# Performance work log

Measured on AMD Instinct MI355X. Metric: run time of the kernel, lower is better.

## Reference

```python
import jax, jax.numpy as jnp
import numpy as np

EMBED_DIM = 512
NUM_HEADS = 8
HEAD_DIM = EMBED_DIM // NUM_HEADS
FFN_DIM = 4 * EMBED_DIM
B, S = 4, 2048
LN_EPS = 1e-5


def _linear_params(key, fan_in, fan_out):
    kw, kb = jax.random.split(key)
    bound = 1.0 / np.sqrt(fan_in)
    W = jax.random.uniform(kw, (fan_in, fan_out), jnp.float32, -bound, bound)
    b = jax.random.uniform(kb, (fan_out,), jnp.float32, -bound, bound)
    return W, b


def setup_inputs() -> dict:
    key = jax.random.key(0)
    ks = jax.random.split(key, 10)
    query = jax.random.normal(ks[0], (B, S, EMBED_DIM), jnp.float32)
    key_t = jax.random.normal(ks[1], (B, S, EMBED_DIM), jnp.float32)
    value = jax.random.normal(ks[2], (B, S, EMBED_DIM), jnp.float32)
    Wq, bq = _linear_params(ks[3], EMBED_DIM, EMBED_DIM)
    Wk, bk = _linear_params(ks[4], EMBED_DIM, EMBED_DIM)
    Wv, bv = _linear_params(ks[5], EMBED_DIM, EMBED_DIM)
    Wo, bo = _linear_params(ks[6], EMBED_DIM, EMBED_DIM)
    W1, b1 = _linear_params(ks[7], EMBED_DIM, FFN_DIM)
    W2, b2 = _linear_params(ks[8], FFN_DIM, EMBED_DIM)
    g1 = jnp.ones((EMBED_DIM,), jnp.float32); be1 = jnp.zeros((EMBED_DIM,), jnp.float32)
    g2 = jnp.ones((EMBED_DIM,), jnp.float32); be2 = jnp.zeros((EMBED_DIM,), jnp.float32)
    return dict(query=query, key=key_t, value=value,
                Wq=Wq, bq=bq, Wk=Wk, bk=bk, Wv=Wv, bv=bv, Wo=Wo, bo=bo,
                g1=g1, be1=be1, g2=g2, be2=be2,
                W1=W1, b1=b1, W2=W2, b2=b2)


def _layernorm(x, g, b):
    mu = jnp.mean(x, axis=-1, keepdims=True)
    var = jnp.mean(jnp.square(x - mu), axis=-1, keepdims=True)
    return (x - mu) * jax.lax.rsqrt(var + LN_EPS) * g + b


def reference(query, key, value, Wq, bq, Wk, bk, Wv, bv, Wo, bo,
              g1, be1, g2, be2, W1, b1, W2, b2):
    b_, s_ = query.shape[:2]
    # projections -> [B, H, S, Dh]
    Q = (query @ Wq + bq).reshape(b_, -1, NUM_HEADS, HEAD_DIM).transpose(0, 2, 1, 3)
    K = (key @ Wk + bk).reshape(b_, -1, NUM_HEADS, HEAD_DIM).transpose(0, 2, 1, 3)
    V = (value @ Wv + bv).reshape(b_, -1, NUM_HEADS, HEAD_DIM).transpose(0, 2, 1, 3)
    scores = jnp.einsum('bhqd,bhkd->bhqk', Q, K) / jnp.sqrt(jnp.float32(HEAD_DIM))
    attn = jax.nn.softmax(scores, axis=-1)  # dropout is eval-mode identity
    ctx = jnp.einsum('bhqk,bhkd->bhqd', attn, V)
    ctx = ctx.transpose(0, 2, 1, 3).reshape(b_, -1, EMBED_DIM)
    out = ctx @ Wo + bo
    out = _layernorm(query + out, g1, be1)
    ffn = jax.nn.gelu(out @ W1 + b1, approximate=False) @ W2 + b2
    return _layernorm(out + ffn, g2, be2)
```

## Files before the change

### kernel.cpp

```cpp
#include <hip/hip_runtime.h>
#include <hip/hip_bf16.h>
#include <math.h>

#define EMBED 512
#define NHEAD 8
#define HDIM 64
#define FFN 2048
#define BB 4
#define SS 2048
#define MROWS (BB*SS)
#define NB ((size_t)MROWS * EMBED)
#define LN_EPS 1e-5f

typedef __attribute__((ext_vector_type(8))) short short8;
typedef __attribute__((ext_vector_type(4))) float floatx4;

__device__ inline float bf2f(__hip_bfloat16 x) { return __bfloat162float(x); }
__device__ inline __hip_bfloat16 f2bf(float x) { return __float2bfloat16(x); }

__device__ inline float gelu_f(float x) {
    return 0.5f * x * (1.0f + erff(x * 0.70710678118654752f));
}

__device__ inline void async_copy16(const void* g, void* l) {
    __builtin_amdgcn_global_load_lds(
        (const __attribute__((address_space(1))) void*)g,
        (__attribute__((address_space(3))) void*)l, 16, 0, 0);
}

__global__ void detect_kernel(const void* __restrict__ q, int* __restrict__ flag) {
    const float* qf = (const float*)q;
    int lane = threadIdx.x;
    float v = qf[lane * 1024 + 7];
    bool ok = (v == v) && (fabsf(v) > 0x1p-40f) && (fabsf(v) < 0x1p40f);
    unsigned long long m = __ballot(ok);
    if (lane == 0) *flag = (__popcll(m) >= 32) ? 1 : 0;
}

__global__ __launch_bounds__(256) void cvt_qkv_kernel(
    const void* __restrict__ q, const void* __restrict__ k, const void* __restrict__ v,
    __hip_bfloat16* __restrict__ out, const int* __restrict__ dflag)
{
    const int f32 = *dflag;
    size_t pos = ((size_t)blockIdx.x * 256 + threadIdx.x) * 8;
    int sel = (int)(pos >> 22);
    size_t off = pos & (NB - 1);
    const void* src = sel == 0 ? q : sel == 1 ? k : v;
    if (f32) {
        const float* s = (const float*)src + off;
        float4 f0 = *reinterpret_cast<const float4*>(s);
        float4 f1 = *reinterpret_cast<const float4*>(s + 4);
        alignas(16) __hip_bfloat16 h[8] = {
            f2bf(f0.x), f2bf(f0.y), f2bf(f0.z), f2bf(f0.w),
            f2bf(f1.x), f2bf(f1.y), f2bf(f1.z), f2bf(f1.w)};
        *reinterpret_cast<uint4*>(out + pos) = *reinterpret_cast<const uint4*>(h);
    } else {
        *reinterpret_cast<uint4*>(out + pos) =
            *reinterpret_cast<const uint4*>((const __hip_bfloat16*)src + off);
    }
}

__global__ __launch_bounds__(256) void transpose_tile_kernel(
    const void* __restrict__ src, __hip_bfloat16* __restrict__ dst,
    int R, int C, const int* __restrict__ dflag)
{
    const int f32 = *dflag;
    const int r0 = blockIdx.x * 64, c0 = blockIdx.y * 64;
    __shared__ __hip_bfloat16 L[64][65];
    const int t = threadIdx.x;
    for (int c = t; c < 4096; c += 256) {
        int lr = c >> 6, lc = c & 63;
        __hip_bfloat16 v = f32 ? f2bf(((const float*)src)[(size_t)(r0 + lr) * C + c0 + lc])
                               : ((const __hip_bfloat16*)src)[(size_t)(r0 + lr) * C + c0 + lc];
        L[lr][lc] = v;
    }
    __syncthreads();
    for (int c = t; c < 4096; c += 256) {
        int lr = c >> 6, lc = c & 63;
        dst[(size_t)(c0 + lr) * R + r0 + lc] = L[lc][lr];
    }
}

__global__ __launch_bounds__(256) void transpose_tile4_kernel(
    const void* __restrict__ s0, const void* __restrict__ s1,
    const void* __restrict__ s2, const void* __restrict__ s3,
    __hip_bfloat16* __restrict__ dbase,
    const int* __restrict__ dflag)
{
    const int f32 = *dflag;
    const int which = blockIdx.z;
    const void* src = which == 0 ? s0 : which == 1 ? s1 : which == 2 ? s2 : s3;
    __hip_bfloat16* dst = dbase + (size_t)which * 512 * 512;
    const int r0 = blockIdx.x * 64, c0 = blockIdx.y * 64;
    __shared__ __hip_bfloat16 L[64][65];
    const int t = threadIdx.x;
    for (int c = t; c < 4096; c += 256) {
        int lr = c >> 6, lc = c & 63;
        __hip_bfloat16 v = f32 ? f2bf(((const float*)src)[(size_t)(r0 + lr) * 512 + c0 + lc])
                               : ((const __hip_bfloat16*)src)[(size_t)(r0 + lr) * 512 + c0 + lc];
        L[lr][lc] = v;
    }
    __syncthreads();
    for (int c = t; c < 4096; c += 256) {
        int lr = c >> 6, lc = c & 63;
        dst[(size_t)(c0 + lr) * 512 + r0 + lc] = L[lc][lr];
    }
}

template<int ACT, int BIAS>
__global__ __launch_bounds__(256) void gemm_bt_lds_kernel(
    const __hip_bfloat16* __restrict__ A,
    const __hip_bfloat16* __restrict__ Bt,
    const void* __restrict__ bias,
    __hip_bfloat16* __restrict__ C,
    int M, int N, int K, int ksplit, const int* __restrict__ dflag)
{
    const int f32 = *dflag;
    const int bm = blockIdx.x * 128;
    const int bn = blockIdx.y * 128;
    int kbeg = 0, kend = K;
    if (BIAS == 0) {
        kbeg = blockIdx.z * ksplit;
        kend = kbeg + ksplit;
        C += (size_t)blockIdx.z * NB;
    }
    const int t = threadIdx.x;
    const int wave = t >> 6, lane = t & 63;
    const int wm = (wave >> 1) * 64, wn = (wave & 1) * 64;
    const int quad = lane >> 4, r = lane & 15;

    __shared__ alignas(16) __hip_bfloat16 As[128 * 32];
    __shared__ alignas(16) __hip_bfloat16 Bs[128 * 32];

    floatx4 acc[4][4];
    #pragma unroll
    for (int i = 0; i < 4; ++i)
        #pragma unroll
        for (int j = 0; j < 4; ++j)
            acc[i][j] = (floatx4){0.f, 0.f, 0.f, 0.f};

    const int c0 = wave * 128;

    for (int kt = kbeg; kt < kend; kt += 32) {
        #pragma unroll
        for (int it = 0; it < 2; ++it) {
            int c = c0 + it * 64 + lane;
            int row = c >> 2, col = (c & 3) * 8;
            async_copy16(A + (size_t)(bm + row) * K + kt + col,
                         As + (size_t)(c0 + it * 64) * 8);
            async_copy16(Bt + (size_t)(bn + row) * K + kt + col,
                         Bs + (size_t)(c0 + it * 64) * 8);
        }
        __syncthreads();
        short8 af[4], bfr[4];
        #pragma unroll
        for (int i = 0; i < 4; ++i)
            af[i] = *reinterpret_cast<const short8*>(&As[(wm + i * 16 + r) * 32 + quad * 8]);
        #pragma unroll
        for (int j = 0; j < 4; ++j)
            bfr[j] = *reinterpret_cast<const short8*>(&Bs[(wn + j * 16 + r) * 32 + quad * 8]);
        #pragma unroll
        for (int i = 0; i < 4; ++i)
            #pragma unroll
            for (int j = 0; j < 4; ++j)
                acc[i][j] = __builtin_amdgcn_mfma_f32_16x16x32_bf16(af[i], bfr[j], acc[i][j], 0, 0, 0);
        __syncthreads();
    }

    #pragma unroll
    for (int j = 0; j < 4; ++j) {
        const int n = bn + wn + j * 16 + r;
        float bvv = 0.f;
        if (BIAS) bvv = f32 ? ((const float*)bias)[n]
                            : bf2f(((const __hip_bfloat16*)bias)[n]);
        #pragma unroll
        for (int i = 0; i < 4; ++i) {
            #pragma unroll
            for (int v = 0; v < 4; ++v) {
                int m = bm + wm + i * 16 + quad * 4 + v;
                float x = acc[i][j][v] + bvv;
                if (ACT == 1) x = gelu_f(x);
                C[(size_t)m * N + n] = f2bf(x);
            }
        }
    }
}

__global__ __launch_bounds__(256) void gemm_qkv_fused_kernel(
    const __hip_bfloat16* __restrict__ Acat,
    const __hip_bfloat16* __restrict__ Wcat,
    const void* __restrict__ bq, const void* __restrict__ bk, const void* __restrict__ bv,
    __hip_bfloat16* __restrict__ Ocat,
    const int* __restrict__ dflag)
{
    const int f32 = *dflag;
    const int sel = blockIdx.x >> 6;
    const __hip_bfloat16* A = Acat + (size_t)sel * NB;
    const __hip_bfloat16* Bt = Wcat + (size_t)sel * 512 * 512;
    const void* bias = sel == 0 ? bq : sel == 1 ? bk : bv;
    __hip_bfloat16* C = Ocat + (size_t)sel * NB;

    const int bm = (blockIdx.x & 63) * 128;
    const int bn = blockIdx.y * 128;
    const int t = threadIdx.x;
    const int wave = t >> 6, lane = t & 63;
    const int wm = (wave >> 1) * 64, wn = (wave & 1) * 64;
    const int quad = lane >> 4, r = lane & 15;
    const int K = EMBED, N = EMBED;

    __shared__ alignas(16) __hip_bfloat16 As[128 * 32];
    __shared__ alignas(16) __hip_bfloat16 Bs[128 * 32];

    floatx4 acc[4][4];
    #pragma unroll
    for (int i = 0; i < 4; ++i)
        #pragma unroll
        for (int j = 0; j < 4; ++j)
            acc[i][j] = (floatx4){0.f, 0.f, 0.f, 0.f};

    const int c0 = wave * 128;

    for (int kt = 0; kt < K; kt += 32) {
        #pragma unroll
        for (int it = 0; it < 2; ++it) {
            int c = c0 + it * 64 + lane;
            int row = c >> 2, col = (c & 3) * 8;
            async_copy16(A + (size_t)(bm + row) * K + kt + col,
                         As + (size_t)(c0 + it * 64) * 8);
            async_copy16(Bt + (size_t)(bn + row) * K + kt + col,
                         Bs + (size_t)(c0 + it * 64) * 8);
        }
        __syncthreads();
        short8 af[4], bfr[4];
        #pragma unroll
        for (int i = 0; i < 4; ++i)
            af[i] = *reinterpret_cast<const short8*>(&As[(wm + i * 16 + r) * 32 + quad * 8]);
        #pragma unroll
        for (int j = 0; j < 4; ++j)
            bfr[j] = *reinterpret_cast<const short8*>(&Bs[(wn + j * 16 + r) * 32 + quad * 8]);
        #pragma unroll
        for (int i = 0; i < 4; ++i)
            #pragma unroll
            for (int j = 0; j < 4; ++j)
                acc[i][j] = __builtin_amdgcn_mfma_f32_16x16x32_bf16(af[i], bfr[j], acc[i][j], 0, 0, 0);
        __syncthreads();
    }

    #pragma unroll
    for (int j = 0; j < 4; ++j) {
        const int n = bn + wn + j * 16 + r;
        const float bvv = f32 ? ((const float*)bias)[n]
                              : bf2f(((const __hip_bfloat16*)bias)[n]);
        #pragma unroll
        for (int i = 0; i < 4; ++i) {
            #pragma unroll
            for (int v = 0; v < 4; ++v) {
                int m = bm + wm + i * 16 + quad * 4 + v;
                C[(size_t)m * N + n] = f2bf(acc[i][j][v] + bvv);
            }
        }
    }
}

__global__ __launch_bounds__(256) void vtrans_kernel(
    const __hip_bfloat16* __restrict__ Vb, __hip_bfloat16* __restrict__ Vt)
{
    const int bh = blockIdx.y;
    const int b = bh >> 3, h = bh & 7;
    const int s0 = blockIdx.x * 64;
    __shared__ alignas(16) __hip_bfloat16 L[64][72];
    const int t = threadIdx.x;
    for (int c = t; c < 512; c += 256) {
        int row = c >> 3, g = c & 7;
        *reinterpret_cast<uint4*>(&L[row][g * 8]) =
            *reinterpret_cast<const uint4*>(Vb + (size_t)(b * SS + s0 + row) * EMBED + h * 64 + g * 8);
    }
    __syncthreads();
    for (int c = t; c < 512; c += 256) {
        int d = c >> 3, g = c & 7;
        alignas(16) __hip_bfloat16 tmp[8];
        #pragma unroll
        for (int j = 0; j < 8; ++j) tmp[j] = L[g * 8 + j][d];
        *reinterpret_cast<uint4*>(Vt + ((size_t)bh * 64 + d) * SS + s0 + g * 8) =
            *reinterpret_cast<const uint4*>(tmp);
    }
}

__global__ __launch_bounds__(256) void attn_mfma_kernel(
    const __hip_bfloat16* __restrict__ Qg,
    const __hip_bfloat16* __restrict__ Kg,
    const __hip_bfloat16* __restrict__ Vt,
    __hip_bfloat16* __restrict__ Apart0,
    __hip_bfloat16* __restrict__ Apart1,
    float2* __restrict__ ml)
{
    const int bh = blockIdx.y;
    const int b = bh >> 3, h = bh & 7;
    const int q0 = blockIdx.x * 64;
    const int z = blockIdx.z;
    const int t = threadIdx.x;
    const int w = t >> 6, lane = t & 63;
    const int quad = lane >> 4, r = lane & 15;

    __shared__ alignas(16) __hip_bfloat16 Ks[2][64 * 32];
    __shared__ alignas(16) __hip_bfloat16 Vs[2][64 * 32];
    __shared__ alignas(16) __hip_bfloat16 Ps[4][16][72];

    const size_t bbase = (size_t)b * SS * EMBED;
    const size_t hoff = (size_t)h * HDIM;
    const size_t vtbase = (size_t)bh * HDIM * SS;

    short8 aq[2];
    {
        const __hip_bfloat16* qrow = Qg + bbase + (size_t)(q0 + w * 16 + r) * EMBED + hoff;
        short8 t0 = *reinterpret_cast<const short8*>(qrow + quad * 8);
        short8 t1 = *reinterpret_cast<const short8*>(qrow + 32 + quad * 8);
        #pragma unroll
        for (int i = 0; i < 8; ++i) {
            ((__hip_bfloat16*)&aq[0])[i] = f2bf(bf2f(((const __hip_bfloat16*)&t0)[i]) * 0.125f);
            ((__hip_bfloat16*)&aq[1])[i] = f2bf(bf2f(((const __hip_bfloat16*)&t1)[i]) * 0.125f);
        }
    }

    const int tensor = w >> 1;
    const int slab = w & 1;
    const int srow = lane >> 2;
    const int scol = (lane & 3) * 8;

    float m_run = -1e30f;
    float l_run = 0.f;
    floatx4 o_acc[4];
    #pragma unroll
    for (int nt = 0; nt < 4; ++nt) o_acc[nt] = (floatx4){0.f, 0.f, 0.f, 0.f};

    const int kbeg = z * (SS / 2), kend = kbeg + SS / 2;
    for (int kt = kbeg; kt < kend; kt += 64) {
        __syncthreads();
        if (tensor == 0) {
            #pragma unroll
            for (int g = 0; g < 4; ++g) {
                int row = g * 16 + srow;
                async_copy16(Kg + bbase + (size_t)(kt + row) * EMBED + hoff + slab * 32 + scol,
                             &Ks[slab][g * 512]);
            }
        } else {
            #pragma unroll
            for (int g = 0; g < 4; ++g) {
                int row = g * 16 + srow;
                async_copy16(Vt + vtbase + (size_t)row * SS + kt + slab * 32 + scol,
                             &Vs[slab][g * 512]);
            }
        }
        __syncthreads();

        floatx4 sc[4];
        #pragma unroll
        for (int nt = 0; nt < 4; ++nt) sc[nt] = (floatx4){0.f, 0.f, 0.f, 0.f};
        #pragma unroll
        for (int nt = 0; nt < 4; ++nt) {
            short8 ak0 = *reinterpret_cast<const short8*>(&Ks[0][(nt * 16 + r) * 32 + quad * 8]);
            short8 ak1 = *reinterpret_cast<const short8*>(&Ks[1][(nt * 16 + r) * 32 + quad * 8]);
            sc[nt] = __builtin_amdgcn_mfma_f32_16x16x32_bf16(ak0, aq[0], sc[nt], 0, 0, 0);
            sc[nt] = __builtin_amdgcn_mfma_f32_16x16x32_bf16(ak1, aq[1], sc[nt], 0, 0, 0);
        }

        float mt = fmaxf(fmaxf(fmaxf(sc[0][0], sc[0][1]), fmaxf(sc[0][2], sc[0][3])),
                         fmaxf(fmaxf(sc[1][0], sc[1][1]), fmaxf(sc[1][2], sc[1][3])));
        mt = fmaxf(mt, fmaxf(fmaxf(fmaxf(sc[2][0], sc[2][1]), fmaxf(sc[2][2], sc[2][3])),
                             fmaxf(fmaxf(sc[3][0], sc[3][1]), fmaxf(sc[3][2], sc[3][3]))));
        mt = fmaxf(mt, __shfl_xor(mt, 16, 64));
        mt = fmaxf(mt, __shfl_xor(mt, 32, 64));

        float mn = fmaxf(m_run, mt);
        float alpha = __expf(m_run - mn);
        m_run = mn;

        float ps = 0.f;
        #pragma unroll
        for (int nt = 0; nt < 4; ++nt) {
            float p0 = __expf(sc[nt][0] - mn), p1 = __expf(sc[nt][1] - mn);
            float p2 = __expf(sc[nt][2] - mn), p3 = __expf(sc[nt][3] - mn);
            ps += (p0 + p1) + (p2 + p3);
            alignas(8) __hip_bfloat16 pk[4] = {f2bf(p0), f2bf(p1), f2bf(p2), f2bf(p3)};
            *reinterpret_cast<uint2*>(&Ps[w][r][nt * 16 + quad * 4]) =
                *reinterpret_cast<const uint2*>(pk);
        }
        ps += __shfl_xor(ps, 16, 64);
        ps += __shfl_xor(ps, 32, 64);
        l_run = l_run * alpha + ps;

        #pragma unroll
        for (int v = 0; v < 4; ++v) {
            float av = __shfl(alpha, quad * 4 + v, 64);
            o_acc[0][v] *= av; o_acc[1][v] *= av;
            o_acc[2][v] *= av; o_acc[3][v] *= av;
        }

        short8 ap0 = *reinterpret_cast<const short8*>(&Ps[w][r][quad * 8]);
        short8 ap1 = *reinterpret_cast<const short8*>(&Ps[w][r][32 + quad * 8]);
        #pragma unroll
        for (int nt = 0; nt < 4; ++nt) {
            short8 bv0 = *reinterpret_cast<const short8*>(&Vs[0][(nt * 16 + r) * 32 + quad * 8]);
            short8 bv1 = *reinterpret_cast<const short8*>(&Vs[1][(nt * 16 + r) * 32 + quad * 8]);
            o_acc[nt] = __builtin_amdgcn_mfma_f32_16x16x32_bf16(ap0, bv0, o_acc[nt], 0, 0, 0);
            o_acc[nt] = __builtin_amdgcn_mfma_f32_16x16x32_bf16(ap1, bv1, o_acc[nt], 0, 0, 0);
        }
    }

    __hip_bfloat16* Ap = z == 0 ? Apart0 : Apart1;
    #pragma unroll
    for (int v = 0; v < 4; ++v) {
        int q = q0 + w * 16 + quad * 4 + v;
        __hip_bfloat16* orow = Ap + bbase + (size_t)q * EMBED + hoff;
        #pragma unroll
        for (int nt = 0; nt < 4; ++nt)
            orow[nt * 16 + r] = f2bf(o_acc[nt][v]);
    }
    if (lane < 16) {
        ml[((size_t)z * 32 + bh) * SS + q0 + w * 16 + r] = make_float2(m_run, l_run);
    }
}

__global__ __launch_bounds__(256) void attn_combine_kernel(
    const __hip_bfloat16* __restrict__ Apart0,
    const __hip_bfloat16* __restrict__ Apart1,
    const float2* __restrict__ ml,
    __hip_bfloat16* __restrict__ ctx)
{
    const int bh = blockIdx.y;
    const int b = bh >> 3, h = bh & 7;
    const int q0 = blockIdx.x * 64;
    const int t = threadIdx.x;
    __shared__ float w0[64], w1[64], winv[64];

    if (t < 64) {
        float2 ml0 = ml[(size_t)bh * SS + q0 + t];
        float2 ml1 = ml[((size_t)32 + bh) * SS + q0 + t];
        float m = fmaxf(ml0.x, ml1.x);
        float a0 = __expf(ml0.x - m), a1 = __expf(ml1.x - m);
        float denom = a0 * ml0.y + a1 * ml1.y;
        w0[t] = a0; w1[t] = a1; winv[t] = 1.0f / denom;
    }
    __syncthreads();

    const size_t base = (size_t)b * SS * EMBED + (size_t)h * HDIM;
    for (int c = t; c < 512; c += 256) {
        int q = c >> 3, d8 = (c & 7) * 8;
        size_t off = base + (size_t)(q0 + q) * EMBED + d8;
        short8 a0v = *reinterpret_cast<const short8*>(Apart0 + off);
        short8 a1v = *reinterpret_cast<const short8*>(Apart1 + off);
        float s0 = w0[q], s1 = w1[q], si = winv[q];
        alignas(16) __hip_bfloat16 o[8];
        #pragma unroll
        for (int j = 0; j < 8; ++j) {
            float x0 = bf2f(((const __hip_bfloat16*)&a0v)[j]);
            float x1 = bf2f(((const __hip_bfloat16*)&a1v)[j]);
            o[j] = f2bf((s0 * x0 + s1 * x1) * si);
        }
        *reinterpret_cast<uint4*>(ctx + off) = *reinterpret_cast<const uint4*>(o);
    }
}

__device__ inline float block_reduce_sum(float v, float* sbuf) {
    #pragma unroll
    for (int off = 32; off; off >>= 1) v += __shfl_xor(v, off, 64);
    int wave = threadIdx.x >> 6;
    if ((threadIdx.x & 63) == 0) sbuf[wave] = v;
    __syncthreads();
    float r = sbuf[0] + sbuf[1] + sbuf[2] + sbuf[3];
    __syncthreads();
    return r;
}

__global__ __launch_bounds__(256) void add_ln_kernel(
    const __hip_bfloat16* __restrict__ X,
    const __hip_bfloat16* __restrict__ Y,
    const void* __restrict__ g,
    const void* __restrict__ bt,
    __hip_bfloat16* __restrict__ out,
    const int* __restrict__ dflag)
{
    __shared__ float sbuf[4];
    const int f32 = *dflag;
    const int row = blockIdx.x;
    const size_t base = (size_t)row * EMBED;
    const int t = threadIdx.x;

    float x0 = bf2f(X[base + t]) + bf2f(Y[base + t]);
    float x1 = bf2f(X[base + t + 256]) + bf2f(Y[base + t + 256]);
    float s = block_reduce_sum(x0 + x1, sbuf);
    float mu = s * (1.0f / EMBED);
    float d0 = x0 - mu, d1 = x1 - mu;
    float vs = block_reduce_sum(d0 * d0 + d1 * d1, sbuf);
    float rstd = rsqrtf(vs * (1.0f / EMBED) + LN_EPS);

    float g0 = f32 ? ((const float*)g)[t]        : bf2f(((const __hip_bfloat16*)g)[t]);
    float g1v = f32 ? ((const float*)g)[t + 256] : bf2f(((const __hip_bfloat16*)g)[t + 256]);
    float b0 = f32 ? ((const float*)bt)[t]        : bf2f(((const __hip_bfloat16*)bt)[t]);
    float b1v = f32 ? ((const float*)bt)[t + 256] : bf2f(((const __hip_bfloat16*)bt)[t + 256]);

    out[base + t]       = f2bf(d0 * rstd * g0 + b0);
    out[base + t + 256] = f2bf(d1 * rstd * g1v + b1v);
}

__global__ __launch_bounds__(256) void add_ln_split_kernel(
    const __hip_bfloat16* __restrict__ X,
    const __hip_bfloat16* __restrict__ Y0,
    const __hip_bfloat16* __restrict__ Y1,
    const void* __restrict__ bias,
    const void* __restrict__ g,
    const void* __restrict__ bt,
    void* __restrict__ out,
    const int* __restrict__ dflag)
{
    __shared__ float sbuf[4];
    const int f32 = *dflag;
    const int row = blockIdx.x;
    const size_t base = (size_t)row * EMBED;
    const int t = threadIdx.x;

    float bb0 = f32 ? ((const float*)bias)[t]       : bf2f(((const __hip_bfloat16*)bias)[t]);
    float bb1 = f32 ? ((const float*)bias)[t + 256] : bf2f(((const __hip_bfloat16*)bias)[t + 256]);
    float x0 = bf2f(X[base + t]) + bf2f(Y0[base + t]) + bf2f(Y1[base + t]) + bb0;
    float x1 = bf2f(X[base + t + 256]) + bf2f(Y0[base + t + 256]) + bf2f(Y1[base + t + 256]) + bb1;
    float s = block_reduce_sum(x0 + x1, sbuf);
    float mu = s * (1.0f / EMBED);
    float d0 = x0 - mu, d1 = x1 - mu;
    float vs = block_reduce_sum(d0 * d0 + d1 * d1, sbuf);
    float rstd = rsqrtf(vs * (1.0f / EMBED) + LN_EPS);

    float g0 = f32 ? ((const float*)g)[t]        : bf2f(((const __hip_bfloat16*)g)[t]);
    float g1v = f32 ? ((const float*)g)[t + 256] : bf2f(((const __hip_bfloat16*)g)[t + 256]);
    float b0 = f32 ? ((const float*)bt)[t]        : bf2f(((const __hip_bfloat16*)bt)[t]);
    float b1v = f32 ? ((const float*)bt)[t + 256] : bf2f(((const __hip_bfloat16*)bt)[t + 256]);

    float o0 = d0 * rstd * g0 + b0;
    float o1 = d1 * rstd * g1v + b1v;
    if (f32) {
        ((float*)out)[base + t] = o0;
        ((float*)out)[base + t + 256] = o1;
    } else {
        ((__hip_bfloat16*)out)[base + t] = f2bf(o0);
        ((__hip_bfloat16*)out)[base + t + 256] = f2bf(o1);
    }
}

extern "C" void kernel_launch(void* const* d_in, const int* in_sizes, int n_in,
                              void* d_out, int out_size, void* d_ws, size_t ws_size,
                              hipStream_t stream)
{
    (void)in_sizes; (void)n_in; (void)out_size; (void)ws_size;

    const void* query = d_in[0];
    const void* keyi  = d_in[1];
    const void* vali  = d_in[2];
    const void* Wq = d_in[3];  const void* bq = d_in[4];
    const void* Wk = d_in[5];  const void* bk = d_in[6];
    const void* Wv = d_in[7];  const void* bv = d_in[8];
    const void* Wo = d_in[9];  const void* bo = d_in[10];
    const void* g1 = d_in[11]; const void* be1 = d_in[12];
    const void* g2 = d_in[13]; const void* be2 = d_in[14];
    const void* W1 = d_in[15]; const void* b1 = d_in[16];
    const void* W2 = d_in[17]; const void* b2 = d_in[18];

    int* dflag = (int*)d_ws;
    __hip_bfloat16* p = (__hip_bfloat16*)((char*)d_ws + 64);
    __hip_bfloat16* WqT = p;
    __hip_bfloat16* WoT = WqT + 3 * 512 * 512;
    __hip_bfloat16* W1T = WoT + 512 * 512;
    __hip_bfloat16* W2T = W1T + 512 * 2048;
    __hip_bfloat16* buf = W2T + 512 * 2048;
    __hip_bfloat16* qkvbf  = buf;
    __hip_bfloat16* QKVo   = buf + 3 * NB;
    __hip_bfloat16* Qb = QKVo;
    __hip_bfloat16* Kb = QKVo + NB;
    __hip_bfloat16* Vb = QKVo + 2 * NB;
    __hip_bfloat16* Vt     = buf + 1 * NB;
    __hip_bfloat16* Apart0 = buf + 2 * NB;
    __hip_bfloat16* Apart1 = buf + 6 * NB;
    float2*         mlbuf  = (float2*)(buf + 7 * NB);
    __hip_bfloat16* ctx    = buf + 3 * NB;
    __hip_bfloat16* prj    = buf + 4 * NB;
    __hip_bfloat16* x1     = buf + 5 * NB;
    __hip_bfloat16* hbf    = buf + 1 * NB;
    __hip_bfloat16* Ypart  = buf + 6 * NB;

    detect_kernel<<<1, 64, 0, stream>>>(query, dflag);

    cvt_qkv_kernel<<<(3 * NB / 8) / 256, 256, 0, stream>>>(query, keyi, vali, qkvbf, dflag);

    transpose_tile4_kernel<<<dim3(8, 8, 4), 256, 0, stream>>>(Wq, Wk, Wv, Wo, WqT, dflag);
    transpose_tile_kernel<<<dim3(8, 32), 256, 0, stream>>>(W1, W1T, 512, 2048, dflag);
    transpose_tile_kernel<<<dim3(32, 8), 256, 0, stream>>>(W2, W2T, 2048, 512, dflag);

    gemm_qkv_fused_kernel<<<dim3(192, 4), 256, 0, stream>>>(qkvbf, WqT, bq, bk, bv, QKVo, dflag);

    vtrans_kernel<<<dim3(SS / 64, BB * NHEAD), 256, 0, stream>>>(Vb, Vt);

    attn_mfma_kernel<<<dim3(SS / 64, BB * NHEAD, 2), 256, 0, stream>>>(
        Qb, Kb, Vt, Apart0, Apart1, mlbuf);
    attn_combine_kernel<<<dim3(SS / 64, BB * NHEAD), 256, 0, stream>>>(
        Apart0, Apart1, mlbuf, ctx);

    gemm_bt_lds_kernel<0, 1><<<dim3(MROWS / 128, EMBED / 128), 256, 0, stream>>>(
        ctx, WoT, bo, prj, MROWS, EMBED, EMBED, 0, dflag);
    add_ln_kernel<<<MROWS, 256, 0, stream>>>(qkvbf, prj, g1, be1, x1, dflag);

    gemm_bt_lds_kernel<1, 1><<<dim3(MROWS / 128, FFN / 128), 256, 0, stream>>>(
        x1, W1T, b1, hbf, MROWS, FFN, EMBED, 0, dflag);
    gemm_bt_lds_kernel<0, 0><<<dim3(MROWS / 128, EMBED / 128, 2), 256, 0, stream>>>(
        hbf, W2T, nullptr, Ypart, MROWS, EMBED, FFN, FFN / 2, dflag);
    add_ln_split_kernel<<<MROWS, 256, 0, stream>>>(
        x1, Ypart, Ypart + NB, b2, g2, be2, d_out, dflag);
}
```

Before: 387.6 us.

## Merge prep kernels, double attention rows per wave, split-K out-projection, exp2 softmax

Replaces the separate input-conversion and weight-transpose launches with a single prep kernel that also converts biases and LayerNorm parameters to bf16 once, so later kernels drop their per-element dtype branches. The attention kernel now handles 128 query rows per block, with each wave processing two 16-row slabs. This reuses every K/V tile in LDS across twice as many queries and halves the grid. Softmax switches to exp2f with log2(e) folded into the Q scale. The output projection becomes a 2-way split-K GEMM whose partial sums are combined in a templated add+LayerNorm kernel, trading more intermediate traffic for extra parallelism. Register pressure in attention rises, which may lower occupancy.

```diff
diff --git a/kernel.cpp b/kernel.cpp
--- a/kernel.cpp
+++ b/kernel.cpp
@@ -11,6 +11,7 @@
 #define MROWS (BB*SS)
 #define NB ((size_t)MROWS * EMBED)
 #define LN_EPS 1e-5f
+#define QSCALE 0.180336880111f
 
 typedef __attribute__((ext_vector_type(8))) short short8;
 typedef __attribute__((ext_vector_type(4))) float floatx4;
@@ -28,51 +29,83 @@
         (__attribute__((address_space(3))) void*)l, 16, 0, 0);
 }
 
+__device__ inline int sane_f(float v) {
+    return (v == v) && (fabsf(v) > 0x1p-40f) && (fabsf(v) < 0x1p40f);
+}
+
 __global__ void detect_kernel(const void* __restrict__ q, int* __restrict__ flag) {
     const float* qf = (const float*)q;
     int lane = threadIdx.x;
     float v = qf[lane * 1024 + 7];
-    bool ok = (v == v) && (fabsf(v) > 0x1p-40f) && (fabsf(v) < 0x1p40f);
+    bool ok = sane_f(v);
     unsigned long long m = __ballot(ok);
     if (lane == 0) *flag = (__popcll(m) >= 32) ? 1 : 0;
 }
 
-__global__ __launch_bounds__(256) void cvt_qkv_kernel(
-    const void* __restrict__ q, const void* __restrict__ k, const void* __restrict__ v,
-    __hip_bfloat16* __restrict__ out, const int* __restrict__ dflag)
-{
-    const int f32 = *dflag;
-    size_t pos = ((size_t)blockIdx.x * 256 + threadIdx.x) * 8;
-    int sel = (int)(pos >> 22);
-    size_t off = pos & (NB - 1);
-    const void* src = sel == 0 ? q : sel == 1 ? k : v;
-    if (f32) {
-        const float* s = (const float*)src + off;
-        float4 f0 = *reinterpret_cast<const float4*>(s);
-        float4 f1 = *reinterpret_cast<const float4*>(s + 4);
-        alignas(16) __hip_bfloat16 h[8] = {
-            f2bf(f0.x), f2bf(f0.y), f2bf(f0.z), f2bf(f0.w),
-            f2bf(f1.x), f2bf(f1.y), f2bf(f1.z), f2bf(f1.w)};
-        *reinterpret_cast<uint4*>(out + pos) = *reinterpret_cast<const uint4*>(h);
+__global__ __launch_bounds__(256) void prep_kernel(
+    const void* __restrict__ query, const void* __restrict__ keyi, const void* __restrict__ vali,
+    const void* __restrict__ Wq, const void* __restrict__ Wk, const void* __restrict__ Wv,
+    const void* __restrict__ Wo, const void* __restrict__ W1, const void* __restrict__ W2,
+    const void* __restrict__ bq, const void* __restrict__ bk, const void* __restrict__ bv,
+    const void* __restrict__ bo, const void* __restrict__ b1, const void* __restrict__ b2,
+    const void* __restrict__ g1, const void* __restrict__ be1,
+    const void* __restrict__ g2, const void* __restrict__ be2,
+    __hip_bfloat16* __restrict__ qkvbf,
+    __hip_bfloat16* __restrict__ Wcat,
+    __hip_bfloat16* __restrict__ biasb)
+{
+    __shared__ __hip_bfloat16 L[64][65];
+    const int f32 = sane_f(((const float*)query)[7]) + sane_f(((const float*)query)[1031]) +
+                    sane_f(((const float*)query)[200003]) + sane_f(((const float*)query)[1000003]) >= 3;
+    const int t = threadIdx.x;
+    const int blk = blockIdx.x;
+
+    if (blk < 6144) {
+        size_t pos = ((size_t)blk * 256 + t) * 8;
+        int sel = (int)(pos >> 22);
+        size_t off = pos & (NB - 1);
+        const void* src = sel == 0 ? query : sel == 1 ? keyi : vali;
+        if (f32) {
+            const float* s = (const float*)src + off;
+            float4 f0 = *reinterpret_cast<const float4*>(s);
+            float4 f1 = *reinterpret_cast<const float4*>(s + 4);
+            alignas(16) __hip_bfloat16 h[8] = {
+                f2bf(f0.x), f2bf(f0.y), f2bf(f0.z), f2bf(f0.w),
+                f2bf(f1.x), f2bf(f1.y), f2bf(f1.z), f2bf(f1.w)};
+            *reinterpret_cast<uint4*>(qkvbf + pos) = *reinterpret_cast<const uint4*>(h);
+        } else {
+            *reinterpret_cast<uint4*>(qkvbf + pos) =
+                *reinterpret_cast<const uint4*>((const __hip_bfloat16*)src + off);
+        }
+        return;
+    }
+
+    const void* src; __hip_bfloat16* dst; int R, C, r0, c0;
+    if (blk < 6400) {
+        int b2i = blk - 6144; src = W1; dst = Wcat + 4 * 512 * 512;
+        R = 512; C = 2048; r0 = (b2i >> 5) * 64; c0 = (b2i & 31) * 64;
+    } else if (blk < 6656) {
+        int b3 = blk - 6400; src = W2; dst = Wcat + 4 * 512 * 512 + 512 * 2048;
+        R = 2048; C = 512; r0 = (b3 >> 3) * 64; c0 = (b3 & 7) * 64;
+    } else if (blk < 6912) {
+        int b4 = blk - 6656; int which = b4 >> 6; int tile = b4 & 63;
+        src = which == 0 ? Wq : which == 1 ? Wk : which == 2 ? Wv : Wo;
+        dst = Wcat + (size_t)which * 512 * 512;
+        R = 512; C = 512; r0 = (tile >> 3) * 64; c0 = (tile & 7) * 64;
     } else {
-        *reinterpret_cast<uint4*>(out + pos) =
-            *reinterpret_cast<const uint4*>((const __hip_bfloat16*)src + off);
-    }
-}
-
-__global__ __launch_bounds__(256) void transpose_tile_kernel(
-    const void* __restrict__ src, __hip_bfloat16* __restrict__ dst,
-    int R, int C, const int* __restrict__ dflag)
-{
-    const int f32 = *dflag;
-    const int r0 = blockIdx.x * 64, c0 = blockIdx.y * 64;
-    __shared__ __hip_bfloat16 L[64][65];
-    const int t = threadIdx.x;
+        const void* srcs[10] = {bq, bk, bv, bo, b1, b2, g1, be1, g2, be2};
+        const int offs[10] = {0, 512, 1024, 1536, 2048, 4096, 4608, 5120, 5632, 6144};
+        const int lens[10] = {512, 512, 512, 512, 2048, 512, 512, 512, 512, 512};
+        for (int a = 0; a < 10; ++a)
+            for (int i = t; i < lens[a]; i += 256)
+                biasb[offs[a] + i] = f32 ? f2bf(((const float*)srcs[a])[i])
+                                         : ((const __hip_bfloat16*)srcs[a])[i];
+        return;
+    }
     for (int c = t; c < 4096; c += 256) {
         int lr = c >> 6, lc = c & 63;
-        __hip_bfloat16 v = f32 ? f2bf(((const float*)src)[(size_t)(r0 + lr) * C + c0 + lc])
-                               : ((const __hip_bfloat16*)src)[(size_t)(r0 + lr) * C + c0 + lc];
-        L[lr][lc] = v;
+        L[lr][lc] = f32 ? f2bf(((const float*)src)[(size_t)(r0 + lr) * C + c0 + lc])
+                        : ((const __hip_bfloat16*)src)[(size_t)(r0 + lr) * C + c0 + lc];
     }
     __syncthreads();
     for (int c = t; c < 4096; c += 256) {
@@ -81,41 +114,14 @@
     }
 }
 
-__global__ __launch_bounds__(256) void transpose_tile4_kernel(
-    const void* __restrict__ s0, const void* __restrict__ s1,
-    const void* __restrict__ s2, const void* __restrict__ s3,
-    __hip_bfloat16* __restrict__ dbase,
-    const int* __restrict__ dflag)
-{
-    const int f32 = *dflag;
-    const int which = blockIdx.z;
-    const void* src = which == 0 ? s0 : which == 1 ? s1 : which == 2 ? s2 : s3;
-    __hip_bfloat16* dst = dbase + (size_t)which * 512 * 512;
-    const int r0 = blockIdx.x * 64, c0 = blockIdx.y * 64;
-    __shared__ __hip_bfloat16 L[64][65];
-    const int t = threadIdx.x;
-    for (int c = t; c < 4096; c += 256) {
-        int lr = c >> 6, lc = c & 63;
-        __hip_bfloat16 v = f32 ? f2bf(((const float*)src)[(size_t)(r0 + lr) * 512 + c0 + lc])
-                               : ((const __hip_bfloat16*)src)[(size_t)(r0 + lr) * 512 + c0 + lc];
-        L[lr][lc] = v;
-    }
-    __syncthreads();
-    for (int c = t; c < 4096; c += 256) {
-        int lr = c >> 6, lc = c & 63;
-        dst[(size_t)(c0 + lr) * 512 + r0 + lc] = L[lc][lr];
-    }
-}
-
 template<int ACT, int BIAS>
 __global__ __launch_bounds__(256) void gemm_bt_lds_kernel(
     const __hip_bfloat16* __restrict__ A,
     const __hip_bfloat16* __restrict__ Bt,
-    const void* __restrict__ bias,
+    const __hip_bfloat16* __restrict__ bias,
     __hip_bfloat16* __restrict__ C,
-    int M, int N, int K, int ksplit, const int* __restrict__ dflag)
-{
-    const int f32 = *dflag;
+    int M, int N, int K, int ksplit)
+{
     const int bm = blockIdx.x * 128;
     const int bn = blockIdx.y * 128;
     int kbeg = 0, kend = K;
@@ -170,9 +176,7 @@
     #pragma unroll
     for (int j = 0; j < 4; ++j) {
         const int n = bn + wn + j * 16 + r;
-        float bvv = 0.f;
-        if (BIAS) bvv = f32 ? ((const float*)bias)[n]
-                            : bf2f(((const __hip_bfloat16*)bias)[n]);
+        float bvv = BIAS ? bf2f(bias[n]) : 0.f;
         #pragma unroll
         for (int i = 0; i < 4; ++i) {
             #pragma unroll
@@ -189,15 +193,13 @@
 __global__ __launch_bounds__(256) void gemm_qkv_fused_kernel(
     const __hip_bfloat16* __restrict__ Acat,
     const __hip_bfloat16* __restrict__ Wcat,
-    const void* __restrict__ bq, const void* __restrict__ bk, const void* __restrict__ bv,
-    __hip_bfloat16* __restrict__ Ocat,
-    const int* __restrict__ dflag)
-{
-    const int f32 = *dflag;
+    const __hip_bfloat16* __restrict__ biascat,
+    __hip_bfloat16* __restrict__ Ocat)
+{
     const int sel = blockIdx.x >> 6;
     const __hip_bfloat16* A = Acat + (size_t)sel * NB;
     const __hip_bfloat16* Bt = Wcat + (size_t)sel * 512 * 512;
-    const void* bias = sel == 0 ? bq : sel == 1 ? bk : bv;
+    const __hip_bfloat16* bias = biascat + sel * 512;
     __hip_bfloat16* C = Ocat + (size_t)sel * NB;
 
     const int bm = (blockIdx.x & 63) * 128;
@@ -249,8 +251,7 @@
     #pragma unroll
     for (int j = 0; j < 4; ++j) {
         const int n = bn + wn + j * 16 + r;
-        const float bvv = f32 ? ((const float*)bias)[n]
-                              : bf2f(((const __hip_bfloat16*)bias)[n]);
+        const float bvv = bf2f(bias[n]);
         #pragma unroll
         for (int i = 0; i < 4; ++i) {
             #pragma unroll
@@ -296,7 +297,7 @@
 {
     const int bh = blockIdx.y;
     const int b = bh >> 3, h = bh & 7;
-    const int q0 = blockIdx.x * 64;
+    const int q0 = blockIdx.x * 128;
     const int z = blockIdx.z;
     const int t = threadIdx.x;
     const int w = t >> 6, lane = t & 63;
@@ -304,34 +305,36 @@
 
     __shared__ alignas(16) __hip_bfloat16 Ks[2][64 * 32];
     __shared__ alignas(16) __hip_bfloat16 Vs[2][64 * 32];
-    __shared__ alignas(16) __hip_bfloat16 Ps[4][16][72];
+    __shared__ alignas(16) __hip_bfloat16 Ps[4][32][72];
 
     const size_t bbase = (size_t)b * SS * EMBED;
     const size_t hoff = (size_t)h * HDIM;
     const size_t vtbase = (size_t)bh * HDIM * SS;
 
-    short8 aq[2];
-    {
-        const __hip_bfloat16* qrow = Qg + bbase + (size_t)(q0 + w * 16 + r) * EMBED + hoff;
+    short8 aq[2][2];
+    #pragma unroll
+    for (int s = 0; s < 2; ++s) {
+        const __hip_bfloat16* qrow = Qg + bbase + (size_t)(q0 + w * 32 + s * 16 + r) * EMBED + hoff;
         short8 t0 = *reinterpret_cast<const short8*>(qrow + quad * 8);
         short8 t1 = *reinterpret_cast<const short8*>(qrow + 32 + quad * 8);
         #pragma unroll
         for (int i = 0; i < 8; ++i) {
-            ((__hip_bfloat16*)&aq[0])[i] = f2bf(bf2f(((const __hip_bfloat16*)&t0)[i]) * 0.125f);
-            ((__hip_bfloat16*)&aq[1])[i] = f2bf(bf2f(((const __hip_bfloat16*)&t1)[i]) * 0.125f);
-        }
-    }
-
-    const int tensor = w >> 1;
-    const int slab = w & 1;
-    const int srow = lane >> 2;
-    const int scol = (lane & 3) * 8;
-
-    float m_run = -1e30f;
-    float l_run = 0.f;
-    floatx4 o_acc[4];
-    #pragma unroll
-    for (int nt = 0; nt < 4; ++nt) o_acc[nt] = (floatx4){0.f, 0.f, 0.f, 0.f};
+            ((__hip_bfloat16*)&aq[s][0])[i] = f2bf(bf2f(((const __hip_bfloat16*)&t0)[i]) * QSCALE);
+            ((__hip_bfloat16*)&aq[s][1])[i] = f2bf(bf2f(((const __hip_bfloat16*)&t1)[i]) * QSCALE);
+        }
+    }
+
+    const int tensor = w >> 1, slab = w & 1;
+    const int srow = lane >> 2, scol = (lane & 3) * 8;
+
+    float m_run[2] = {-1e30f, -1e30f};
+    float l_run[2] = {0.f, 0.f};
+    floatx4 o0[4], o1[4];
+    #pragma unroll
+    for (int nt = 0; nt < 4; ++nt) {
+        o0[nt] = (floatx4){0.f, 0.f, 0.f, 0.f};
+        o1[nt] = (floatx4){0.f, 0.f, 0.f, 0.f};
+    }
 
     const int kbeg = z * (SS / 2), kend = kbeg + SS / 2;
     for (int kt = kbeg; kt < kend; kt += 64) {
@@ -353,71 +356,92 @@
         }
         __syncthreads();
 
-        floatx4 sc[4];
-        #pragma unroll
-        for (int nt = 0; nt < 4; ++nt) sc[nt] = (floatx4){0.f, 0.f, 0.f, 0.f};
+        floatx4 s0[4], s1[4];
+        #pragma unroll
+        for (int nt = 0; nt < 4; ++nt) {
+            s0[nt] = (floatx4){0.f, 0.f, 0.f, 0.f};
+            s1[nt] = (floatx4){0.f, 0.f, 0.f, 0.f};
+        }
         #pragma unroll
         for (int nt = 0; nt < 4; ++nt) {
             short8 ak0 = *reinterpret_cast<const short8*>(&Ks[0][(nt * 16 + r) * 32 + quad * 8]);
             short8 ak1 = *reinterpret_cast<const short8*>(&Ks[1][(nt * 16 + r) * 32 + quad * 8]);
-            sc[nt] = __builtin_amdgcn_mfma_f32_16x16x32_bf16(ak0, aq[0], sc[nt], 0, 0, 0);
-            sc[nt] = __builtin_amdgcn_mfma_f32_16x16x32_bf16(ak1, aq[1], sc[nt], 0, 0, 0);
-        }
-
-        float mt = fmaxf(fmaxf(fmaxf(sc[0][0], sc[0][1]), fmaxf(sc[0][2], sc[0][3])),
-                         fmaxf(fmaxf(sc[1][0], sc[1][1]), fmaxf(sc[1][2], sc[1][3])));
-        mt = fmaxf(mt, fmaxf(fmaxf(fmaxf(sc[2][0], sc[2][1]), fmaxf(sc[2][2], sc[2][3])),
-                             fmaxf(fmaxf(sc[3][0], sc[3][1]), fmaxf(sc[3][2], sc[3][3]))));
-        mt = fmaxf(mt, __shfl_xor(mt, 16, 64));
-        mt = fmaxf(mt, __shfl_xor(mt, 32, 64));
-
-        float mn = fmaxf(m_run, mt);
-        float alpha = __expf(m_run - mn);
-        m_run = mn;
-
-        float ps = 0.f;
-        #pragma unroll
-        for (int nt = 0; nt < 4; ++nt) {
-            float p0 = __expf(sc[nt][0] - mn), p1 = __expf(sc[nt][1] - mn);
-            float p2 = __expf(sc[nt][2] - mn), p3 = __expf(sc[nt][3] - mn);
-            ps += (p0 + p1) + (p2 + p3);
-            alignas(8) __hip_bfloat16 pk[4] = {f2bf(p0), f2bf(p1), f2bf(p2), f2bf(p3)};
-            *reinterpret_cast<uint2*>(&Ps[w][r][nt * 16 + quad * 4]) =
-                *reinterpret_cast<const uint2*>(pk);
-        }
-        ps += __shfl_xor(ps, 16, 64);
-        ps += __shfl_xor(ps, 32, 64);
-        l_run = l_run * alpha + ps;
+            s0[nt] = __builtin_amdgcn_mfma_f32_16x16x32_bf16(ak0, aq[0][0], s0[nt], 0, 0, 0);
+            s0[nt] = __builtin_amdgcn_mfma_f32_16x16x32_bf16(ak1, aq[0][1], s0[nt], 0, 0, 0);
+            s1[nt] = __builtin_amdgcn_mfma_f32_16x16x32_bf16(ak0, aq[1][0], s1[nt], 0, 0, 0);
+            s1[nt] = __builtin_amdgcn_mfma_f32_16x16x32_bf16(ak1, aq[1][1], s1[nt], 0, 0, 0);
+        }
+
+        float alpha[2];
+        #pragma unroll
+        for (int s = 0; s < 2; ++s) {
+            floatx4* sc = s == 0 ? s0 : s1;
+            float mt = fmaxf(fmaxf(fmaxf(sc[0][0], sc[0][1]), fmaxf(sc[0][2], sc[0][3])),
+                             fmaxf(fmaxf(sc[1][0], sc[1][1]), fmaxf(sc[1][2], sc[1][3])));
+            mt = fmaxf(mt, fmaxf(fmaxf(fmaxf(sc[2][0], sc[2][1]), fmaxf(sc[2][2], sc[2][3])),
+                                 fmaxf(fmaxf(sc[3][0], sc[3][1]), fmaxf(sc[3][2], sc[3][3]))));
+            mt = fmaxf(mt, __shfl_xor(mt, 16, 64));
+            mt = fmaxf(mt, __shfl_xor(mt, 32, 64));
+            float mn = fmaxf(m_run[s], mt);
+            alpha[s] = exp2f(m_run[s] - mn);
+            m_run[s] = mn;
+            float ps = 0.f;
+            #pragma unroll
+            for (int nt = 0; nt < 4; ++nt) {
+                float p0 = exp2f(sc[nt][0] - mn), p1 = exp2f(sc[nt][1] - mn);
+                float p2 = exp2f(sc[nt][2] - mn), p3 = exp2f(sc[nt][3] - mn);
+                ps += (p0 + p1) + (p2 + p3);
+                __hip_bfloat162 pa = __float22bfloat162_rn(make_float2(p0, p1));
+                __hip_bfloat162 pb = __float22bfloat162_rn(make_float2(p2, p3));
+                uint2 u;
+                u.x = *reinterpret_cast<unsigned*>(&pa);
+                u.y = *reinterpret_cast<unsigned*>(&pb);
+                *reinterpret_cast<uint2*>(&Ps[w][s * 16 + r][nt * 16 + quad * 4]) = u;
+            }
+            ps += __shfl_xor(ps, 16, 64);
+            ps += __shfl_xor(ps, 32, 64);
+            l_run[s] = l_run[s] * alpha[s] + ps;
+        }
 
         #pragma unroll
         for (int v = 0; v < 4; ++v) {
-            float av = __shfl(alpha, quad * 4 + v, 64);
-            o_acc[0][v] *= av; o_acc[1][v] *= av;
-            o_acc[2][v] *= av; o_acc[3][v] *= av;
-        }
-
-        short8 ap0 = *reinterpret_cast<const short8*>(&Ps[w][r][quad * 8]);
-        short8 ap1 = *reinterpret_cast<const short8*>(&Ps[w][r][32 + quad * 8]);
+            float a0 = __shfl(alpha[0], quad * 4 + v, 64);
+            float a1 = __shfl(alpha[1], quad * 4 + v, 64);
+            #pragma unroll
+            for (int nt = 0; nt < 4; ++nt) { o0[nt][v] *= a0; o1[nt][v] *= a1; }
+        }
+
+        short8 ap00 = *reinterpret_cast<const short8*>(&Ps[w][r][quad * 8]);
+        short8 ap01 = *reinterpret_cast<const short8*>(&Ps[w][r][32 + quad * 8]);
+        short8 ap10 = *reinterpret_cast<const short8*>(&Ps[w][16 + r][quad * 8]);
+        short8 ap11 = *reinterpret_cast<const short8*>(&Ps[w][16 + r][32 + quad * 8]);
         #pragma unroll
         for (int nt = 0; nt < 4; ++nt) {
             short8 bv0 = *reinterpret_cast<const short8*>(&Vs[0][(nt * 16 + r) * 32 + quad * 8]);
             short8 bv1 = *reinterpret_cast<const short8*>(&Vs[1][(nt * 16 + r) * 32 + quad * 8]);
-            o_acc[nt] = __builtin_amdgcn_mfma_f32_16x16x32_bf16(ap0, bv0, o_acc[nt], 0, 0, 0);
-            o_acc[nt] = __builtin_amdgcn_mfma_f32_16x16x32_bf16(ap1, bv1, o_acc[nt], 0, 0, 0);
+            o0[nt] = __builtin_amdgcn_mfma_f32_16x16x32_bf16(ap00, bv0, o0[nt], 0, 0, 0);
+            o0[nt] = __builtin_amdgcn_mfma_f32_16x16x32_bf16(ap01, bv1, o0[nt], 0, 0, 0);
+            o1[nt] = __builtin_amdgcn_mfma_f32_16x16x32_bf16(ap10, bv0, o1[nt], 0, 0, 0);
+            o1[nt] = __builtin_amdgcn_mfma_f32_16x16x32_bf16(ap11, bv1, o1[nt], 0, 0, 0);
         }
     }
 
     __hip_bfloat16* Ap = z == 0 ? Apart0 : Apart1;
     #pragma unroll
-    for (int v = 0; v < 4; ++v) {
-        int q = q0 + w * 16 + quad * 4 + v;
-        __hip_bfloat16* orow = Ap + bbase + (size_t)q * EMBED + hoff;
-        #pragma unroll
-        for (int nt = 0; nt < 4; ++nt)
-            orow[nt * 16 + r] = f2bf(o_acc[nt][v]);
-    }
-    if (lane < 16) {
-        ml[((size_t)z * 32 + bh) * SS + q0 + w * 16 + r] = make_float2(m_run, l_run);
+    for (int s = 0; s < 2; ++s) {
+        floatx4* oa = s == 0 ? o0 : o1;
+        #pragma unroll
+        for (int v = 0; v < 4; ++v) {
+            int q = q0 + w * 32 + s * 16 + quad * 4 + v;
+            __hip_bfloat16* orow = Ap + bbase + (size_t)q * EMBED + hoff;
+            #pragma unroll
+            for (int nt = 0; nt < 4; ++nt)
+                orow[nt * 16 + r] = f2bf(oa[nt][v]);
+        }
+    }
+    if (lane < 32) {
+        int s = lane >> 4;
+        ml[((size_t)z * 32 + bh) * SS + q0 + w * 32 + lane] = make_float2(m_run[s], l_run[s]);
     }
 }
 
@@ -437,7 +461,7 @@
         float2 ml0 = ml[(size_t)bh * SS + q0 + t];
         float2 ml1 = ml[((size_t)32 + bh) * SS + q0 + t];
         float m = fmaxf(ml0.x, ml1.x);
-        float a0 = __expf(ml0.x - m), a1 = __expf(ml1.x - m);
+        float a0 = exp2f(ml0.x - m), a1 = exp2f(ml1.x - m);
         float denom = a0 * ml0.y + a1 * ml1.y;
         w0[t] = a0; w1[t] = a1; winv[t] = 1.0f / denom;
     }
@@ -472,71 +496,33 @@
     return r;
 }
 
-__global__ __launch_bounds__(256) void add_ln_kernel(
+template<int OUT32>
+__global__ __launch_bounds__(256) void add_ln_split_kernel(
     const __hip_bfloat16* __restrict__ X,
-    const __hip_bfloat16* __restrict__ Y,
-    const void* __restrict__ g,
-    const void* __restrict__ bt,
-    __hip_bfloat16* __restrict__ out,
+    const __hip_bfloat16* __restrict__ Y0,
+    const __hip_bfloat16* __restrict__ Y1,
+    const __hip_bfloat16* __restrict__ bias,
+    const __hip_bfloat16* __restrict__ g,
+    const __hip_bfloat16* __restrict__ bt,
+    void* __restrict__ out,
     const int* __restrict__ dflag)
 {
     __shared__ float sbuf[4];
-    const int f32 = *dflag;
     const int row = blockIdx.x;
     const size_t base = (size_t)row * EMBED;
     const int t = threadIdx.x;
 
-    float x0 = bf2f(X[base + t]) + bf2f(Y[base + t]);
-    float x1 = bf2f(X[base + t + 256]) + bf2f(Y[base + t + 256]);
+    float x0 = bf2f(X[base + t]) + bf2f(Y0[base + t]) + bf2f(Y1[base + t]) + bf2f(bias[t]);
+    float x1 = bf2f(X[base + t + 256]) + bf2f(Y0[base + t + 256]) + bf2f(Y1[base + t + 256]) + bf2f(bias[t + 256]);
     float s = block_reduce_sum(x0 + x1, sbuf);
     float mu = s * (1.0f / EMBED);
     float d0 = x0 - mu, d1 = x1 - mu;
     float vs = block_reduce_sum(d0 * d0 + d1 * d1, sbuf);
     float rstd = rsqrtf(vs * (1.0f / EMBED) + LN_EPS);
 
-    float g0 = f32 ? ((const float*)g)[t]        : bf2f(((const __hip_bfloat16*)g)[t]);
-    float g1v = f32 ? ((const float*)g)[t + 256] : bf2f(((const __hip_bfloat16*)g)[t + 256]);
-    float b0 = f32 ? ((const float*)bt)[t]        : bf2f(((const __hip_bfloat16*)bt)[t]);
-    float b1v = f32 ? ((const float*)bt)[t + 256] : bf2f(((const __hip_bfloat16*)bt)[t + 256]);
-
-    out[base + t]       = f2bf(d0 * rstd * g0 + b0);
-    out[base + t + 256] = f2bf(d1 * rstd * g1v + b1v);
-}
-
-__global__ __launch_bounds__(256) void add_ln_split_kernel(
-    const __hip_bfloat16* __restrict__ X,
-    const __hip_bfloat16* __restrict__ Y0,
-    const __hip_bfloat16* __restrict__ Y1,
-    const void* __restrict__ bias,
-    const void* __restrict__ g,
-    const void* __restrict__ bt,
-    void* __restrict__ out,
-    const int* __restrict__ dflag)
-{
-    __shared__ float sbuf[4];
-    const int f32 = *dflag;
-    const int row = blockIdx.x;
-    const size_t base = (size_t)row * EMBED;
-    const int t = threadIdx.x;
-
-    float bb0 = f32 ? ((const float*)bias)[t]       : bf2f(((const __hip_bfloat16*)bias)[t]);
-    float bb1 = f32 ? ((const float*)bias)[t + 256] : bf2f(((const __hip_bfloat16*)bias)[t + 256]);
-    float x0 = bf2f(X[base + t]) + bf2f(Y0[base + t]) + bf2f(Y1[base + t]) + bb0;
-    float x1 = bf2f(X[base + t + 256]) + bf2f(Y0[base + t + 256]) + bf2f(Y1[base + t + 256]) + bb1;
-    float s = block_reduce_sum(x0 + x1, sbuf);
-    float mu = s * (1.0f / EMBED);
-    float d0 = x0 - mu, d1 = x1 - mu;
-    float vs = block_reduce_sum(d0 * d0 + d1 * d1, sbuf);
-    float rstd = rsqrtf(vs * (1.0f / EMBED) + LN_EPS);
-
-    float g0 = f32 ? ((const float*)g)[t]        : bf2f(((const __hip_bfloat16*)g)[t]);
-    float g1v = f32 ? ((const float*)g)[t + 256] : bf2f(((const __hip_bfloat16*)g)[t + 256]);
-    float b0 = f32 ? ((const float*)bt)[t]        : bf2f(((const __hip_bfloat16*)bt)[t]);
-    float b1v = f32 ? ((const float*)bt)[t + 256] : bf2f(((const __hip_bfloat16*)bt)[t + 256]);
-
-    float o0 = d0 * rstd * g0 + b0;
-    float o1 = d1 * rstd * g1v + b1v;
-    if (f32) {
+    float o0 = d0 * rstd * bf2f(g[t]) + bf2f(bt[t]);
+    float o1 = d1 * rstd * bf2f(g[t + 256]) + bf2f(bt[t + 256]);
+    if (OUT32 && *dflag) {
         ((float*)out)[base + t] = o0;
         ((float*)out)[base + t + 256] = o1;
     } else {
@@ -564,12 +550,17 @@
     const void* W2 = d_in[17]; const void* b2 = d_in[18];
 
     int* dflag = (int*)d_ws;
-    __hip_bfloat16* p = (__hip_bfloat16*)((char*)d_ws + 64);
-    __hip_bfloat16* WqT = p;
-    __hip_bfloat16* WoT = WqT + 3 * 512 * 512;
-    __hip_bfloat16* W1T = WoT + 512 * 512;
-    __hip_bfloat16* W2T = W1T + 512 * 2048;
-    __hip_bfloat16* buf = W2T + 512 * 2048;
+    __hip_bfloat16* biasb = (__hip_bfloat16*)((char*)d_ws + 64);
+    __hip_bfloat16* Wcat = biasb + 8192;
+    __hip_bfloat16* buf = Wcat + 4 * 512 * 512 + 2 * 512 * 2048;
+    __hip_bfloat16* bqkvb = biasb;
+    __hip_bfloat16* bob  = biasb + 1536;
+    __hip_bfloat16* b1b  = biasb + 2048;
+    __hip_bfloat16* b2b  = biasb + 4096;
+    __hip_bfloat16* g1b  = biasb + 4608;
+    __hip_bfloat16* be1b = biasb + 5120;
+    __hip_bfloat16* g2b  = biasb + 5632;
+    __hip_bfloat16* be2b = biasb + 6144;
     __hip_bfloat16* qkvbf  = buf;
     __hip_bfloat16* QKVo   = buf + 3 * NB;
     __hip_bfloat16* Qb = QKVo;
@@ -580,36 +571,36 @@
     __hip_bfloat16* Apart1 = buf + 6 * NB;
     float2*         mlbuf  = (float2*)(buf + 7 * NB);
     __hip_bfloat16* ctx    = buf + 3 * NB;
-    __hip_bfloat16* prj    = buf + 4 * NB;
-    __hip_bfloat16* x1     = buf + 5 * NB;
-    __hip_bfloat16* hbf    = buf + 1 * NB;
-    __hip_bfloat16* Ypart  = buf + 6 * NB;
+    __hip_bfloat16* Yw     = buf + 4 * NB;
+    __hip_bfloat16* x1     = buf + 3 * NB;
+    __hip_bfloat16* hbf    = buf + 4 * NB;
+    __hip_bfloat16* Yf     = buf + 1 * NB;
 
     detect_kernel<<<1, 64, 0, stream>>>(query, dflag);
 
-    cvt_qkv_kernel<<<(3 * NB / 8) / 256, 256, 0, stream>>>(query, keyi, vali, qkvbf, dflag);
-
-    transpose_tile4_kernel<<<dim3(8, 8, 4), 256, 0, stream>>>(Wq, Wk, Wv, Wo, WqT, dflag);
-    transpose_tile_kernel<<<dim3(8, 32), 256, 0, stream>>>(W1, W1T, 512, 2048, dflag);
-    transpose_tile_kernel<<<dim3(32, 8), 256, 0, stream>>>(W2, W2T, 2048, 512, dflag);
-
-    gemm_qkv_fused_kernel<<<dim3(192, 4), 256, 0, stream>>>(qkvbf, WqT, bq, bk, bv, QKVo, dflag);
+    prep_kernel<<<6913, 256, 0, stream>>>(
+        query, keyi, vali, Wq, Wk, Wv, Wo, W1, W2,
+        bq, bk, bv, bo, b1, b2, g1, be1, g2, be2,
+        qkvbf, Wcat, biasb);
+
+    gemm_qkv_fused_kernel<<<dim3(192, 4), 256, 0, stream>>>(qkvbf, Wcat, bqkvb, QKVo);
 
     vtrans_kernel<<<dim3(SS / 64, BB * NHEAD), 256, 0, stream>>>(Vb, Vt);
 
-    attn_mfma_kernel<<<dim3(SS / 64, BB * NHEAD, 2), 256, 0, stream>>>(
+    attn_mfma_kernel<<<dim3(SS / 128, BB * NHEAD, 2), 256, 0, stream>>>(
         Qb, Kb, Vt, Apart0, Apart1, mlbuf);
     attn_combine_kernel<<<dim3(SS / 64, BB * NHEAD), 256, 0, stream>>>(
         Apart0, Apart1, mlbuf, ctx);
 
-    gemm_bt_lds_kernel<0, 1><<<dim3(MROWS / 128, EMBED / 128), 256, 0, stream>>>(
-        ctx, WoT, bo, prj, MROWS, EMBED, EMBED, 0, dflag);
-    add_ln_kernel<<<MROWS, 256, 0, stream>>>(qkvbf, prj, g1, be1, x1, dflag);
+    gemm_bt_lds_kernel<0, 0><<<dim3(MROWS / 128, EMBED / 128, 2), 256, 0, stream>>>(
+        ctx, Wcat + 3 * 512 * 512, nullptr, Yw, MROWS, EMBED, EMBED, EMBED / 2);
+    add_ln_split_kernel<0><<<MROWS, 256, 0, stream>>>(
+        qkvbf, Yw, Yw + NB, bob, g1b, be1b, x1, dflag);
 
     gemm_bt_lds_kernel<1, 1><<<dim3(MROWS / 128, FFN / 128), 256, 0, stream>>>(
-        x1, W1T, b1, hbf, MROWS, FFN, EMBED, 0, dflag);
+        x1, Wcat + 4 * 512 * 512, b1b, hbf, MROWS, FFN, EMBED, 0);
     gemm_bt_lds_kernel<0, 0><<<dim3(MROWS / 128, EMBED / 128, 2), 256, 0, stream>>>(
-        hbf, W2T, nullptr, Ypart, MROWS, EMBED, FFN, FFN / 2, dflag);
-    add_ln_split_kernel<<<MROWS, 256, 0, stream>>>(
-        x1, Ypart, Ypart + NB, b2, g2, be2, d_out, dflag);
-}
+        hbf, Wcat + 4 * 512 * 512 + 512 * 2048, nullptr, Yf, MROWS, EMBED, FFN, FFN / 2);
+    add_ln_split_kernel<1><<<MROWS, 256, 0, stream>>>(
+        x1, Yf, Yf + NB, b2b, g2b, be2b, d_out, dflag);
+}
```

Measured after the change: 369.0 us. 4.8% less time.
